# Performance work log

Hardware: AMD Instinct MI355X
Metric: run time of the kernel (lower is better)

## Reference

```python
import jax, jax.numpy as jnp
import numpy as np


def _l2_normalize(v, axis, eps=1e-12):
    # matches F.normalize / cosine_similarity denominator clamping
    n = jnp.linalg.norm(v, axis=axis, keepdims=True)
    return v / jnp.maximum(n, eps)


def setup_inputs() -> dict:
    key = jax.random.key(0)
    k1, k2, k3 = jax.random.split(key, 3)
    B, D, C = 65536, 1024, 4
    x = jax.random.normal(k1, (B, D), dtype=jnp.float32)
    label = jax.random.randint(k2, (B,), 0, C, dtype=jnp.int64)
    text_concept = jax.random.normal(k3, (C, D), dtype=jnp.float32)
    concept_flag = 2
    return {"x": x, "label": label, "text_concept": text_concept, "concept_flag": concept_flag}


def reference(x, label, text_concept, concept_flag):
    B = x.shape[0]
    x = x.reshape(B, x.shape[1])
    # F.normalize(x, dim=1); cosine_similarity then re-normalizes (idempotent for x)
    xn = _l2_normalize(x, axis=1)            # [B, D]
    tn = _l2_normalize(text_concept, axis=1)  # [4, D]
    # per-sample: sim = cos(x_i, text_concept)  -> batched matmul [B, 4]
    sim = jnp.einsum('bd,cd->bc', xn, tn)
    # exp(sim[flag]) / sum(exp(sim)) == softmax over concepts, pick flag column
    probs = jax.nn.softmax(sim, axis=1)      # [B, 4]
    loss = jnp.mean(probs[:, concept_flag])
    return loss
```

## Files before the change

### kernel.cpp

```cpp
#include <hip/hip_runtime.h>
#include <math.h>

#define B_ROWS 65536
#define DIM    1024
#define NCON   4
#define NBLK   1024

__global__ void norm_tc_kernel(const float* __restrict__ tc, float* __restrict__ tn) {
    const int wid  = threadIdx.x >> 6;
    const int lane = threadIdx.x & 63;
    const float* row = tc + wid * DIM;

    float4 v[4];
    float ss = 0.f;
#pragma unroll
    for (int it = 0; it < 4; ++it) {
        v[it] = *reinterpret_cast<const float4*>(row + it * 256 + lane * 4);
        ss += v[it].x * v[it].x + v[it].y * v[it].y + v[it].z * v[it].z + v[it].w * v[it].w;
    }
#pragma unroll
    for (int m = 32; m >= 1; m >>= 1) ss += __shfl_xor(ss, m);
    const float inv = 1.f / fmaxf(sqrtf(ss), 1e-12f);
#pragma unroll
    for (int it = 0; it < 4; ++it) {
        float4 o = make_float4(v[it].x * inv, v[it].y * inv, v[it].z * inv, v[it].w * inv);
        *reinterpret_cast<float4*>(tn + wid * DIM + it * 256 + lane * 4) = o;
    }
}

__global__ void __launch_bounds__(256) sim_kernel(const float* __restrict__ x,
                                                  const float* __restrict__ tn,
                                                  const int*   __restrict__ flag_ptr,
                                                  float*       __restrict__ partials) {
    const int wid  = threadIdx.x >> 6;
    const int lane = threadIdx.x & 63;
    const int gw   = blockIdx.x * 4 + wid;
    const int nw   = NBLK * 4;

    float4 t[NCON][4];
#pragma unroll
    for (int c = 0; c < NCON; ++c)
#pragma unroll
        for (int it = 0; it < 4; ++it)
            t[c][it] = *reinterpret_cast<const float4*>(tn + c * DIM + it * 256 + lane * 4);

    const int flag = *flag_ptr;

    float wsum = 0.f;
    for (int r = gw; r < B_ROWS; r += nw) {
        const float* xr = x + (size_t)r * DIM;
        float4 xv[4];
#pragma unroll
        for (int it = 0; it < 4; ++it)
            xv[it] = *reinterpret_cast<const float4*>(xr + it * 256 + lane * 4);

        float acc0 = 0.f, acc1 = 0.f, acc2 = 0.f, acc3 = 0.f, xx = 0.f;
#pragma unroll
        for (int it = 0; it < 4; ++it) {
            const float4 v = xv[it];
            xx += v.x * v.x + v.y * v.y + v.z * v.z + v.w * v.w;
            acc0 += v.x * t[0][it].x + v.y * t[0][it].y + v.z * t[0][it].z + v.w * t[0][it].w;
            acc1 += v.x * t[1][it].x + v.y * t[1][it].y + v.z * t[1][it].z + v.w * t[1][it].w;
            acc2 += v.x * t[2][it].x + v.y * t[2][it].y + v.z * t[2][it].z + v.w * t[2][it].w;
            acc3 += v.x * t[3][it].x + v.y * t[3][it].y + v.z * t[3][it].z + v.w * t[3][it].w;
        }
#pragma unroll
        for (int m = 32; m >= 1; m >>= 1) {
            xx   += __shfl_xor(xx,   m);
            acc0 += __shfl_xor(acc0, m);
            acc1 += __shfl_xor(acc1, m);
            acc2 += __shfl_xor(acc2, m);
            acc3 += __shfl_xor(acc3, m);
        }
        if (lane == 0) {
            const float inv = 1.f / fmaxf(sqrtf(xx), 1e-12f);
            const float s0 = acc0 * inv, s1 = acc1 * inv, s2 = acc2 * inv, s3 = acc3 * inv;
            const float mx = fmaxf(fmaxf(s0, s1), fmaxf(s2, s3));
            const float e0 = __expf(s0 - mx), e1 = __expf(s1 - mx),
                        e2 = __expf(s2 - mx), e3 = __expf(s3 - mx);
            const float esum = e0 + e1 + e2 + e3;
            const float sel  = (flag == 0) ? e0 : (flag == 1) ? e1 : (flag == 2) ? e2 : e3;
            wsum += sel / esum;
        }
    }

    __shared__ float ls[4];
    if (lane == 0) ls[wid] = wsum;
    __syncthreads();
    if (threadIdx.x == 0) partials[blockIdx.x] = ls[0] + ls[1] + ls[2] + ls[3];
}

__global__ void reduce_kernel(const float* __restrict__ partials, float* __restrict__ out) {
    __shared__ double ls[256];
    double s = 0.0;
    for (int i = threadIdx.x; i < NBLK; i += 256) s += (double)partials[i];
    ls[threadIdx.x] = s;
    __syncthreads();
    for (int st = 128; st >= 1; st >>= 1) {
        if (threadIdx.x < st) ls[threadIdx.x] += ls[threadIdx.x + st];
        __syncthreads();
    }
    if (threadIdx.x == 0) out[0] = (float)(ls[0] / (double)B_ROWS);
}

extern "C" void kernel_launch(void* const* d_in, const int* in_sizes, int n_in,
                              void* d_out, int out_size, void* d_ws, size_t ws_size,
                              hipStream_t stream) {
    const float* x    = (const float*)d_in[0];
    const float* tc   = (const float*)d_in[2];
    const int*   flag = (const int*)d_in[3];
    float* out = (float*)d_out;

    float* tn       = (float*)d_ws;
    float* partials = tn + NCON * DIM;

    norm_tc_kernel<<<1, 256, 0, stream>>>(tc, tn);
    sim_kernel<<<NBLK, 256, 0, stream>>>(x, tn, flag, partials);
    reduce_kernel<<<1, 256, 0, stream>>>(partials, out);
}
```

Before: 52.64 us.

## Fuse concept normalization into sim kernel and software-pipeline row loads

Drops the separate text-concept normalization kernel; each wave now loads and normalizes the 4 concept rows itself, which removes one launch and its dependency. The row loop is rewritten with a fixed trip count and register double-buffering, so the next row's x loads are issued before the current row is computed. A launch_bounds occupancy hint is also added. In exchange, every wave redundantly recomputes the concept norms, and the extra buffered registers raise register pressure.

```diff
diff --git a/kernel.cpp b/kernel.cpp
--- a/kernel.cpp
+++ b/kernel.cpp
@@ -6,59 +6,59 @@
 #define NCON   4
 #define NBLK   1024
 
-__global__ void norm_tc_kernel(const float* __restrict__ tc, float* __restrict__ tn) {
+__global__ void __launch_bounds__(256, 4) sim_kernel(const float* __restrict__ x,
+                                                     const float* __restrict__ tc,
+                                                     const int*   __restrict__ flag_ptr,
+                                                     float*       __restrict__ partials) {
     const int wid  = threadIdx.x >> 6;
     const int lane = threadIdx.x & 63;
-    const float* row = tc + wid * DIM;
-
-    float4 v[4];
-    float ss = 0.f;
-#pragma unroll
-    for (int it = 0; it < 4; ++it) {
-        v[it] = *reinterpret_cast<const float4*>(row + it * 256 + lane * 4);
-        ss += v[it].x * v[it].x + v[it].y * v[it].y + v[it].z * v[it].z + v[it].w * v[it].w;
-    }
-#pragma unroll
-    for (int m = 32; m >= 1; m >>= 1) ss += __shfl_xor(ss, m);
-    const float inv = 1.f / fmaxf(sqrtf(ss), 1e-12f);
-#pragma unroll
-    for (int it = 0; it < 4; ++it) {
-        float4 o = make_float4(v[it].x * inv, v[it].y * inv, v[it].z * inv, v[it].w * inv);
-        *reinterpret_cast<float4*>(tn + wid * DIM + it * 256 + lane * 4) = o;
-    }
-}
-
-__global__ void __launch_bounds__(256) sim_kernel(const float* __restrict__ x,
-                                                  const float* __restrict__ tn,
-                                                  const int*   __restrict__ flag_ptr,
-                                                  float*       __restrict__ partials) {
-    const int wid  = threadIdx.x >> 6;
-    const int lane = threadIdx.x & 63;
-    const int gw   = blockIdx.x * 4 + wid;
-    const int nw   = NBLK * 4;
 
     float4 t[NCON][4];
 #pragma unroll
-    for (int c = 0; c < NCON; ++c)
+    for (int c = 0; c < NCON; ++c) {
+        float ss = 0.f;
 #pragma unroll
-        for (int it = 0; it < 4; ++it)
-            t[c][it] = *reinterpret_cast<const float4*>(tn + c * DIM + it * 256 + lane * 4);
+        for (int it = 0; it < 4; ++it) {
+            t[c][it] = *reinterpret_cast<const float4*>(tc + c * DIM + it * 256 + lane * 4);
+            ss += t[c][it].x * t[c][it].x + t[c][it].y * t[c][it].y
+                + t[c][it].z * t[c][it].z + t[c][it].w * t[c][it].w;
+        }
+#pragma unroll
+        for (int m = 32; m >= 1; m >>= 1) ss += __shfl_xor(ss, m);
+        const float inv = 1.f / fmaxf(sqrtf(ss), 1e-12f);
+#pragma unroll
+        for (int it = 0; it < 4; ++it) {
+            t[c][it].x *= inv; t[c][it].y *= inv; t[c][it].z *= inv; t[c][it].w *= inv;
+        }
+    }
 
     const int flag = *flag_ptr;
 
+    constexpr int ROWS_PER_WAVE = B_ROWS / (NBLK * 4);
+    const int    gw      = blockIdx.x * 4 + wid;
+    const size_t rstride = (size_t)(NBLK * 4) * DIM;
+    const float* xr      = x + (size_t)gw * DIM + lane * 4;
+
+    float4 cur[4], nxt[4];
+#pragma unroll
+    for (int it = 0; it < 4; ++it)
+        cur[it] = *reinterpret_cast<const float4*>(xr + it * 256);
+
     float wsum = 0.f;
-    for (int r = gw; r < B_ROWS; r += nw) {
-        const float* xr = x + (size_t)r * DIM;
-        float4 xv[4];
+#pragma unroll 2
+    for (int i = 0; i < ROWS_PER_WAVE; ++i) {
+        if (i + 1 < ROWS_PER_WAVE) {
+            const float* xn = xr + (size_t)(i + 1) * rstride;
 #pragma unroll
-        for (int it = 0; it < 4; ++it)
-            xv[it] = *reinterpret_cast<const float4*>(xr + it * 256 + lane * 4);
+            for (int it = 0; it < 4; ++it)
+                nxt[it] = *reinterpret_cast<const float4*>(xn + it * 256);
+        }
 
         float acc0 = 0.f, acc1 = 0.f, acc2 = 0.f, acc3 = 0.f, xx = 0.f;
 #pragma unroll
         for (int it = 0; it < 4; ++it) {
-            const float4 v = xv[it];
-            xx += v.x * v.x + v.y * v.y + v.z * v.z + v.w * v.w;
+            const float4 v = cur[it];
+            xx   += v.x * v.x        + v.y * v.y        + v.z * v.z        + v.w * v.w;
             acc0 += v.x * t[0][it].x + v.y * t[0][it].y + v.z * t[0][it].z + v.w * t[0][it].w;
             acc1 += v.x * t[1][it].x + v.y * t[1][it].y + v.z * t[1][it].z + v.w * t[1][it].w;
             acc2 += v.x * t[2][it].x + v.y * t[2][it].y + v.z * t[2][it].z + v.w * t[2][it].w;
@@ -81,6 +81,11 @@
             const float esum = e0 + e1 + e2 + e3;
             const float sel  = (flag == 0) ? e0 : (flag == 1) ? e1 : (flag == 2) ? e2 : e3;
             wsum += sel / esum;
+        }
+
+        if (i + 1 < ROWS_PER_WAVE) {
+#pragma unroll
+            for (int it = 0; it < 4; ++it) cur[it] = nxt[it];
         }
     }
 
@@ -111,10 +116,8 @@
     const int*   flag = (const int*)d_in[3];
     float* out = (float*)d_out;
 
-    float* tn       = (float*)d_ws;
-    float* partials = tn + NCON * DIM;
+    float* partials = (float*)d_ws;
 
-    norm_tc_kernel<<<1, 256, 0, stream>>>(tc, tn);
-    sim_kernel<<<NBLK, 256, 0, stream>>>(x, tn, flag, partials);
+    sim_kernel<<<NBLK, 256, 0, stream>>>(x, tc, flag, partials);
     reduce_kernel<<<1, 256, 0, stream>>>(partials, out);
 }
```

New measurement: 49.61 us. -5.7%, faster.
